# Optimization experiments

Hardware: AMD Instinct MI355X
Metric: run time of the kernel (lower is better)

The kernel has to match this reference:

```python
import jax, jax.numpy as jnp
import numpy as np

K_REP = 4          # repulsion neighbors
REP_THRESH = 0.02  # repulsion distance threshold
K_NORM = 16        # PCA-normal neighborhood size (includes self)
CD_W, REP_W, NORM_W = 1.0, 0.1, 0.01


def _pdist2(x, y):
    # squared pairwise distances: [B,N,M]
    xx = (x * x).sum(-1)
    yy = (y * y).sum(-1)
    return xx[..., :, None] + yy[..., None, :] - 2.0 * jnp.einsum('bnd,bmd->bnm', x, y)


def _gather_points(pts, idx):
    # pts: [B,N,3], idx: [B,N,k] -> [B,N,k,3]
    return jax.vmap(lambda p, i: p[i])(pts, idx)


def _pca_normals(pts):
    # normals via PCA over K_NORM nearest neighbors (self included)
    D = _pdist2(pts, pts)                       # [B,N,N]
    _, idx = jax.lax.top_k(-D, K_NORM)          # [B,N,K]
    nb = _gather_points(pts, idx)               # [B,N,K,3]
    c = nb - nb.mean(axis=-2, keepdims=True)
    cov = jnp.einsum('bnkd,bnke->bnde', c, c) / K_NORM  # [B,N,3,3]
    _, vecs = jnp.linalg.eigh(cov)              # ascending eigenvalues
    return vecs[..., :, 0]                      # eigenvector of smallest eigenvalue


def reference(pred, gt):
    # --- chamfer distance (squared, bidirectional mean) ---
    Dpg = _pdist2(pred, gt)                     # [B,N,M]
    cd = Dpg.min(axis=-1).mean() + Dpg.min(axis=-2).mean()

    # --- repulsion loss: k=4 NN on pred (excluding self) ---
    Dpp = _pdist2(pred, pred)                   # [B,N,N]
    neg_d2, _ = jax.lax.top_k(-Dpp, K_REP + 1)  # nearest incl. self
    d2 = -neg_d2[..., 1:]                       # drop self
    d = jnp.sqrt(jnp.maximum(d2, 1e-12))
    rep = jax.nn.relu(REP_THRESH - d).mean()

    # --- normal consistency via PCA normals (k=16) ---
    n_pred = _pca_normals(pred)
    n_gt = _pca_normals(gt)
    normc = 1.0 - (n_pred * n_gt).sum(-1).mean()

    return CD_W * cd + REP_W * rep + NORM_W * normc


def setup_inputs() -> dict:
    key = jax.random.key(0)
    k1, k2 = jax.random.split(key)
    B, N = 8, 2048
    pred = jax.random.uniform(k1, (B, N, 3), dtype=jnp.float32)
    gt = jax.random.uniform(k2, (B, N, 3), dtype=jnp.float32)
    return {"pred": pred, "gt": gt}
```

## Files before the change

kernel.cpp:

```cpp
#include <hip/hip_runtime.h>


#define NB 8
#define NP 2048
#define KW 10
#define KN 16
#define NQ (2 * NB * NP)


__device__ __forceinline__ float f_slapy2(float x, float y) {
    float xa = fabsf(x), ya = fabsf(y);
    float w = fmaxf(xa, ya), zm = fminf(xa, ya);
    if (zm == 0.f) return w;
    float q = zm / w;
    return w * sqrtf(1.f + q * q);
}

__device__ __forceinline__ void f_slartg(float f, float g, float* cs, float* sn, float* r) {
    if (g == 0.f) { *cs = 1.f; *sn = 0.f; *r = f; }
    else if (f == 0.f) { *cs = 0.f; *sn = copysignf(1.f, g); *r = fabsf(g); }
    else {
        float d = sqrtf(__fadd_rn(__fmul_rn(f, f), __fmul_rn(g, g)));
        *cs = fabsf(f) / d;
        *r  = copysignf(d, f);
        *sn = g / *r;
    }
}

__device__ void f_slaev2(float a, float b, float c,
                         float* rt1, float* rt2, float* cs1, float* sn1) {
    float sm = a + c;
    float df = a - c;
    float adf = fabsf(df);
    float tb = b + b;
    float ab = fabsf(tb);
    float acmx, acmn;
    if (fabsf(a) > fabsf(c)) { acmx = a; acmn = c; } else { acmx = c; acmn = a; }
    float rt;
    if (adf > ab)      { float q = ab / adf; rt = adf * sqrtf(1.f + q * q); }
    else if (adf < ab) { float q = adf / ab; rt = ab * sqrtf(1.f + q * q); }
    else               rt = ab * sqrtf(2.f);
    int sgn1;
    if (sm < 0.f) {
        *rt1 = 0.5f * (sm - rt); sgn1 = -1;
        *rt2 = (acmx / *rt1) * acmn - (b / *rt1) * b;
    } else if (sm > 0.f) {
        *rt1 = 0.5f * (sm + rt); sgn1 = 1;
        *rt2 = (acmx / *rt1) * acmn - (b / *rt1) * b;
    } else {
        *rt1 = 0.5f * rt; *rt2 = -0.5f * rt; sgn1 = 1;
    }
    float cs; int sgn2;
    if (df >= 0.f) { cs = df + rt; sgn2 = 1; }
    else           { cs = df - rt; sgn2 = -1; }
    float acs = fabsf(cs);
    if (acs > ab) {
        float ct = -tb / cs;
        *sn1 = 1.f / sqrtf(1.f + ct * ct);
        *cs1 = ct * *sn1;
    } else {
        if (ab == 0.f) { *cs1 = 1.f; *sn1 = 0.f; }
        else {
            float tn = -cs / tb;
            *cs1 = 1.f / sqrtf(1.f + tn * tn);
            *sn1 = tn * *cs1;
        }
    }
    if (sgn1 == sgn2) { float tn = *cs1; *cs1 = -*sn1; *sn1 = tn; }
}


__device__ __forceinline__ float get3(float a, float b, float c, int i) {
    return i == 0 ? a : (i == 1 ? b : c);
}
__device__ __forceinline__ void set3(float& a, float& b, float& c, int i, float v) {
    a = (i == 0) ? v : a;
    b = (i == 1) ? v : b;
    c = (i == 2) ? v : c;
}
__device__ __forceinline__ float get2(float a, float b, int i) { return i == 0 ? a : b; }
__device__ __forceinline__ void set2(float& a, float& b, int i, float v) {
    a = (i == 0) ? v : a;
    b = (i == 1) ? v : b;
}

#define DGET(i)    get3(dd0, dd1, dd2, (i))
#define DSET(i, v) set3(dd0, dd1, dd2, (i), (v))
#define EGET(i)    get2(ee0, ee1, (i))
#define ESET(i, v) set2(ee0, ee1, (i), (v))
#define ZGET(r, c)    get3(z##r##0, z##r##1, z##r##2, (c))
#define ZSET(r, c, v) set3(z##r##0, z##r##1, z##r##2, (c), (v))
#define ZROT(r, ca, cb, cc, ss) { float zt_ = ZGET(r, (ca)); float zb_ = ZGET(r, (cb)); \
    ZSET(r, (ca), (cc) * zt_ - (ss) * zb_); ZSET(r, (cb), (ss) * zt_ + (cc) * zb_); }
#define ZROT3(ca, cb, cc, ss) { ZROT(0, (ca), (cb), (cc), (ss)) ZROT(1, (ca), (cb), (cc), (ss)) ZROT(2, (ca), (cb), (cc), (ss)) }

__device__ void ssyevd3_evec0(float a00, float a10, float a20,
                              float a11, float a21, float a22,
                              float* ox, float* oy, float* oz) {
    float dd0, dd1, dd2, ee0, ee1;
    float tau = 0.f, v2 = 0.f;
    float xnorm = fabsf(a20);
    if (xnorm == 0.f) {
        tau = 0.f;
        dd0 = a00; dd1 = a11; dd2 = a22; ee0 = a10; ee1 = a21;
    } else {
        float beta = -copysignf(f_slapy2(a10, xnorm), a10);
        tau = (beta - a10) / beta;
        float inv = 1.f / (a10 - beta);
        v2 = a20 * inv;
        float x1 = tau * (a11 + a21 * v2);
        float x2 = tau * (a21 + a22 * v2);
        float alpha = -0.5f * tau * (x1 + x2 * v2);
        float w1 = x1 + alpha;
        float w2 = x2 + alpha * v2;
        float b11 = a11 - 2.f * w1;
        float b21 = a21 - v2 * w1 - w2;
        float b22 = a22 - 2.f * (v2 * w2);
        dd0 = a00; dd1 = b11; dd2 = b22; ee0 = beta; ee1 = b21;
    }
    const float eps    = 5.9604645e-08f;
    const float eps2   = eps * eps;
    const float safmin = 1.1754944e-38f;
    const float ssfmax = sqrtf(1.f / safmin) / 3.f;
    const float ssfmin = sqrtf(safmin) / eps2;
    const int n = 3, nmaxit = 90;
    float z00 = 1.f, z01 = 0.f, z02 = 0.f;
    float z10 = 0.f, z11 = 1.f, z12 = 0.f;
    float z20 = 0.f, z21 = 0.f, z22 = 1.f;
    int jtot = 0;
    int l1 = 1;

    while (true) {
        if (l1 > n) break;
        if (l1 > 1) ESET(l1 - 2, 0.f);
        int m = n;
        {
            bool found = false;
            #pragma unroll
            for (int mi = 1; mi <= 2; ++mi) {
                if (!found && mi >= l1) {
                    float tst = fabsf(EGET(mi - 1));
                    if (tst == 0.f) { m = mi; found = true; }
                    else if (tst <= (sqrtf(fabsf(DGET(mi - 1))) * sqrtf(fabsf(DGET(mi)))) * eps) {
                        ESET(mi - 1, 0.f); m = mi; found = true;
                    }
                }
            }
        }
        int l = l1, lsv = l, lend = m, lendsv = lend;
        l1 = m + 1;
        if (lend == l) continue;

        float anorm = 0.f;
        #pragma unroll
        for (int i = 1; i <= 3; ++i)
            if (i >= l && i <= lend) anorm = fmaxf(anorm, fabsf(DGET(i - 1)));
        #pragma unroll
        for (int i = 1; i <= 2; ++i)
            if (i >= l && i <= lend - 1) anorm = fmaxf(anorm, fabsf(EGET(i - 1)));
        int iscale = 0; float sclto = 1.f;
        if (anorm == 0.f) continue;
        if (anorm > ssfmax) { iscale = 1; sclto = ssfmax; }
        else if (anorm < ssfmin) { iscale = 2; sclto = ssfmin; }
        if (iscale) {
            float mul = sclto / anorm;
            #pragma unroll
            for (int i = 1; i <= 3; ++i)
                if (i >= l && i <= lend) DSET(i - 1, DGET(i - 1) * mul);
            #pragma unroll
            for (int i = 1; i <= 2; ++i)
                if (i >= l && i <= lend - 1) ESET(i - 1, EGET(i - 1) * mul);
        }
        if (fabsf(DGET(lend - 1)) < fabsf(DGET(l - 1))) { lend = lsv; l = lendsv; }

        if (lend > l) {
            while (true) {
                int mq = lend;
                if (l != lend) {
                    bool found = false;
                    #pragma unroll
                    for (int i = 1; i <= 2; ++i) {
                        if (!found && i >= l && i <= lend - 1) {
                            float ei = EGET(i - 1);
                            float tst = ei * ei;
                            if (tst <= (eps2 * fabsf(DGET(i - 1))) * fabsf(DGET(i)) + safmin) { mq = i; found = true; }
                        }
                    }
                }
                if (mq < lend) ESET(mq - 1, 0.f);
                float p = DGET(l - 1);
                if (mq == l) { DSET(l - 1, p); l = l + 1; if (l <= lend) continue; break; }
                if (mq == l + 1) {
                    float rt1, rt2, c, s;
                    f_slaev2(DGET(l - 1), EGET(l - 1), DGET(l), &rt1, &rt2, &c, &s);
                    ZROT3(l, l - 1, c, s);
                    DSET(l - 1, rt1); DSET(l, rt2); ESET(l - 1, 0.f);
                    l += 2; if (l <= lend) continue; break;
                }
                if (jtot == nmaxit) break;
                jtot++;
                float g = (DGET(l) - p) / (2.f * EGET(l - 1));
                float r = f_slapy2(g, 1.f);
                g = DGET(mq - 1) - p + EGET(l - 1) / (g + copysignf(r, g));
                float s = 1.f, c = 1.f; p = 0.f;
                float cw0 = 0.f, cw1 = 0.f, sw0 = 0.f, sw1 = 0.f;
                #pragma unroll
                for (int i = 2; i >= 1; --i) {
                    if (i <= mq - 1 && i >= l) {
                        float f = s * EGET(i - 1);
                        float b = c * EGET(i - 1);
                        f_slartg(g, f, &c, &s, &r);
                        if (i != mq - 1) ESET(i, r);
                        g = DGET(i) - p;
                        r = (DGET(i - 1) - g) * s + 2.f * c * b;
                        p = s * r;
                        DSET(i, g + p);
                        g = c * r - b;
                        set2(cw0, cw1, i - l, c);
                        set2(sw0, sw1, i - l, -s);
                    }
                }
                #pragma unroll
                for (int j = 2; j >= 1; --j) {
                    if (j <= mq - l) {
                        float cj = get2(cw0, cw1, j - 1), sj = get2(sw0, sw1, j - 1);
                        int c0 = l - 1 + (j - 1);
                        ZROT3(c0 + 1, c0, cj, sj);
                    }
                }
                DSET(l - 1, DGET(l - 1) - p);
                ESET(l - 1, g);
            }
        } else {
            while (true) {
                int mq = lend;
                if (l != lend) {
                    bool found = false;
                    #pragma unroll
                    for (int i = 3; i >= 2; --i) {
                        if (!found && i <= l && i >= lend + 1) {
                            float ei = EGET(i - 2);
                            float tst = ei * ei;
                            if (tst <= (eps2 * fabsf(DGET(i - 1))) * fabsf(DGET(i - 2)) + safmin) { mq = i; found = true; }
                        }
                    }
                }
                if (mq > lend) ESET(mq - 2, 0.f);
                float p = DGET(l - 1);
                if (mq == l) { DSET(l - 1, p); l = l - 1; if (l >= lend) continue; break; }
                if (mq == l - 1) {
                    float rt1, rt2, c, s;
                    f_slaev2(DGET(l - 2), EGET(l - 2), DGET(l - 1), &rt1, &rt2, &c, &s);
                    ZROT3(l - 1, l - 2, c, s);
                    DSET(l - 2, rt1); DSET(l - 1, rt2); ESET(l - 2, 0.f);
                    l -= 2; if (l >= lend) continue; break;
                }
                if (jtot == nmaxit) break;
                jtot++;
                float g = (DGET(l - 2) - p) / (2.f * EGET(l - 2));
                float r = f_slapy2(g, 1.f);
                g = DGET(mq - 1) - p + EGET(l - 2) / (g + copysignf(r, g));
                float s = 1.f, c = 1.f; p = 0.f;
                float cw0 = 0.f, cw1 = 0.f, sw0 = 0.f, sw1 = 0.f;
                #pragma unroll
                for (int i = 1; i <= 2; ++i) {
                    if (i >= mq && i <= l - 1) {
                        float f = s * EGET(i - 1);
                        float b = c * EGET(i - 1);
                        f_slartg(g, f, &c, &s, &r);
                        if (i != mq) ESET(i - 2, r);
                        g = DGET(i - 1) - p;
                        r = (DGET(i) - g) * s + 2.f * c * b;
                        p = s * r;
                        DSET(i - 1, g + p);
                        g = c * r - b;
                        set2(cw0, cw1, i - mq, c);
                        set2(sw0, sw1, i - mq, s);
                    }
                }
                #pragma unroll
                for (int j = 1; j <= 2; ++j) {
                    if (j <= l - mq) {
                        float cj = get2(cw0, cw1, j - 1), sj = get2(sw0, sw1, j - 1);
                        int c0 = mq - 1 + (j - 1);
                        ZROT3(c0 + 1, c0, cj, sj);
                    }
                }
                DSET(l - 1, DGET(l - 1) - p);
                ESET(l - 2, g);
            }
        }
        if (iscale) {
            float mul = anorm / sclto;
            #pragma unroll
            for (int i = 1; i <= 3; ++i)
                if (i >= lsv && i <= lendsv) DSET(i - 1, DGET(i - 1) * mul);
            #pragma unroll
            for (int i = 1; i <= 2; ++i)
                if (i >= lsv && i <= lendsv - 1) ESET(i - 1, EGET(i - 1) * mul);
        }
        if (jtot >= nmaxit) break;
    }

    #pragma unroll
    for (int ii = 2; ii <= 3; ++ii) {
        int i = ii - 1, k = i;
        float p = DGET(i - 1);
        #pragma unroll
        for (int j = ii; j <= 3; ++j)
            if (DGET(j - 1) < p) { k = j; p = DGET(j - 1); }
        if (k != i) {
            DSET(k - 1, DGET(i - 1)); DSET(i - 1, p);
            { float t0 = ZGET(0, i - 1); ZSET(0, i - 1, ZGET(0, k - 1)); ZSET(0, k - 1, t0); }
            { float t1 = ZGET(1, i - 1); ZSET(1, i - 1, ZGET(1, k - 1)); ZSET(1, k - 1, t1); }
            { float t2 = ZGET(2, i - 1); ZSET(2, i - 1, ZGET(2, k - 1)); ZSET(2, k - 1, t2); }
        }
    }
    float r0 = z00, r1 = z10, r2 = z20;
    if (tau != 0.f) {
        float sum = r1 + v2 * r2;
        r1 -= tau * sum;
        r2 -= tau * (v2 * sum);
    }
    *ox = r0; *oy = r1; *oz = r2;
}


__device__ __forceinline__ float dot_rn(float ax, float ay, float az,
                                        float bx, float by, float bz) {
    return __fadd_rn(__fadd_rn(__fmul_rn(ax, bx), __fmul_rn(ay, by)), __fmul_rn(az, bz));
}

__device__ __forceinline__ void chain10(unsigned k[KW], unsigned x) {
    unsigned t = x;
    #pragma unroll
    for (int s = 0; s < KW; ++s) {
        unsigned lo = k[s] < t ? k[s] : t;
        unsigned hi = k[s] < t ? t : k[s];
        k[s] = lo; t = hi;
    }
}
__device__ __forceinline__ void chain16(unsigned k[KN], unsigned x) {
    unsigned t = x;
    #pragma unroll
    for (int s = 0; s < KN; ++s) {
        unsigned lo = k[s] < t ? k[s] : t;
        unsigned hi = k[s] < t ? t : k[s];
        k[s] = lo; t = hi;
    }
}

__global__ __launch_bounds__(512, 4) void scan_kernel(
    const float* __restrict__ pred, const float* __restrict__ gt,
    unsigned* __restrict__ kbuf_g, float* __restrict__ mbuf_g)
{
    __shared__ float4 sHome[NP];
    __shared__ float4 sOther[NP];

    int bi = blockIdx.x;
    bool predHome = bi < NB * 32;
    int lb = predHome ? bi : bi - NB * 32;
    int b = lb >> 5;
    int tile = lb & 31;
    int tid  = threadIdx.x;
    int wave = tid >> 6;
    int lane = tid & 63;

    const float* home  = (predHome ? pred : gt) + (size_t)b * NP * 3;
    const float* other = (predHome ? gt : pred) + (size_t)b * NP * 3;

    for (int t = tid; t < NP; t += 512) {
        float hx = home[3 * t], hy = home[3 * t + 1], hz = home[3 * t + 2];
        sHome[t] = make_float4(hx, hy, hz, dot_rn(hx, hy, hz, hx, hy, hz));
        float ox = other[3 * t], oy = other[3 * t + 1], oz = other[3 * t + 2];
        sOther[t] = make_float4(ox, oy, oz, 0.f);
    }
    __syncthreads();

    int im = tile * 64 + lane;
    float4 qv = sHome[im];
    float qx = qv.x, qy = qv.y, qz = qv.z, qq = qv.w;

    unsigned keys[KW];
    #pragma unroll
    for (int s = 0; s < KW; ++s) keys[s] = 0x7F800000u | (unsigned)s;

    float minv = 1e30f;

    for (int t = 0; t < NP / 8; ++t) {
        int jj = (t << 3) | wave;
        float4 h = sHome[jj];
        float dotj = dot_rn(qx, qy, qz, h.x, h.y, h.z);
        float d2 = __fsub_rn(__fadd_rn(qq, h.w), __fmul_rn(2.f, dotj));
        chain10(keys, (__float_as_uint(d2) & 0xFFFFF800u) | (unsigned)jj);
        float4 o = sOther[jj];
        float ex = qx - o.x, ey = qy - o.y, ez = qz - o.z;
        minv = fminf(minv, fmaf(ex, ex, fmaf(ey, ey, ez * ez)));
    }

    size_t gq = (size_t)(predHome ? 0 : NB * NP) + (size_t)b * NP + im;
    #pragma unroll
    for (int s = 0; s < KW; ++s)
        kbuf_g[(size_t)(s * 8 + wave) * NQ + gq] = keys[s];
    mbuf_g[(size_t)wave * NQ + gq] = minv;
}

__global__ __launch_bounds__(1024, 4) void tail_kernel(
    const float* __restrict__ pred, const float* __restrict__ gt,
    const unsigned* __restrict__ kbuf_g, const float* __restrict__ mbuf_g,
    float* __restrict__ normals, double* __restrict__ cdpart)
{
    __shared__ double wsum[16];
    int tid = threadIdx.x;
    int wave = tid >> 6, lane = tid & 63;
    size_t gq = (size_t)blockIdx.x * 1024 + tid;

    bool predHome = gq < (size_t)(NB * NP);
    int gi = predHome ? (int)gq : (int)(gq - NB * NP);
    int b  = gi >> 11;
    int im = gi & (NP - 1);
    const float* home = (predHome ? pred : gt) + (size_t)b * NP * 3;

    float qx = home[3 * im], qy = home[3 * im + 1], qz = home[3 * im + 2];
    float qq = dot_rn(qx, qy, qz, qx, qy, qz);

    unsigned k16[KN];
    unsigned tenth[8];
    #pragma unroll
    for (int s = 0; s < KW; ++s) k16[s] = kbuf_g[(size_t)(s * 8 + 0) * NQ + gq];
    tenth[0] = k16[KW - 1];
    #pragma unroll
    for (int s = KW; s < KN; ++s) k16[s] = 0x7F800000u | (unsigned)s;

    unsigned kc[KW], kn[KW];
    #pragma unroll
    for (int s = 0; s < KW; ++s) kc[s] = kbuf_g[(size_t)(s * 8 + 1) * NQ + gq];
    #pragma unroll
    for (int w = 1; w < 8; ++w) {
        if (w < 7) {
            #pragma unroll
            for (int s = 0; s < KW; ++s) kn[s] = kbuf_g[(size_t)(s * 8 + (w + 1)) * NQ + gq];
        }
        tenth[w] = kc[KW - 1];
        #pragma unroll
        for (int s = 0; s < KW; ++s) {
            unsigned kk = kc[s];
            if (__any(kk < k16[KN - 1])) chain16(k16, kk);
        }
        if (w < 7) {
            #pragma unroll
            for (int s = 0; s < KW; ++s) kc[s] = kn[s];
        }
    }
    float minv = fminf(fminf(fminf(mbuf_g[0 * NQ + gq], mbuf_g[1 * NQ + gq]),
                             fminf(mbuf_g[2 * NQ + gq], mbuf_g[3 * NQ + gq])),
                       fminf(fminf(mbuf_g[4 * NQ + gq], mbuf_g[5 * NQ + gq]),
                             fminf(mbuf_g[6 * NQ + gq], mbuf_g[7 * NQ + gq])));

    unsigned flags = 0;
    #pragma unroll
    for (int w = 0; w < 8; ++w)
        flags |= (tenth[w] < k16[KN - 1]) ? (1u << w) : 0u;

    if (__any(flags != 0)) {
        #pragma unroll
        for (int s = 0; s < KN; ++s)
            k16[s] = flags ? (0x7F800000u | (unsigned)s) : k16[s];
        for (int w = 0; w < 8; ++w) {
            #pragma unroll
            for (int s = 0; s < KW; ++s) {
                unsigned kk = kbuf_g[(size_t)(s * 8 + w) * NQ + gq];
                bool use = (flags != 0) && !((flags >> w) & 1);
                chain16(k16, use ? kk : 0xFFFFFFFFu);
            }
        }
        for (int w = 0; w < 8; ++w) {
            if (__any((flags >> w) & 1)) {
                bool actw = ((flags >> w) & 1) != 0;
                for (int t = 0; t < NP / 8; ++t) {
                    int jj = (t << 3) | w;
                    float hx = home[3 * jj], hy = home[3 * jj + 1], hz = home[3 * jj + 2];
                    float hw = dot_rn(hx, hy, hz, hx, hy, hz);
                    float dotj = dot_rn(qx, qy, qz, hx, hy, hz);
                    float d2 = __fsub_rn(__fadd_rn(qq, hw), __fmul_rn(2.f, dotj));
                    unsigned key = (__float_as_uint(d2) & 0xFFFFF800u) | (unsigned)jj;
                    chain16(k16, actw ? key : 0xFFFFFFFFu);
                }
            }
        }
    }

    float rep = 0.0f;
    if (predHome) {
        #pragma unroll
        for (int r = 1; r <= 4; ++r) {
            float d2 = __uint_as_float(k16[r] & 0xFFFFF800u);
            float dd = sqrtf(fmaxf(d2, 1e-12f));
            rep += fmaxf(0.02f - dd, 0.0f);
        }
    }

    float sx = 0.f, sy = 0.f, sz = 0.f;
    #pragma unroll
    for (int s = 0; s < KN; ++s) {
        const float* hp = home + 3 * (size_t)(k16[s] & 0x7FFu);
        sx += hp[0]; sy += hp[1]; sz += hp[2];
    }
    float mx = sx * (1.0f / KN), my = sy * (1.0f / KN), mz = sz * (1.0f / KN);
    float cxx = 0.f, cxy = 0.f, cxz = 0.f, cyy = 0.f, cyz = 0.f, czz = 0.f;
    #pragma unroll
    for (int s = 0; s < KN; ++s) {
        const float* hp = home + 3 * (size_t)(k16[s] & 0x7FFu);
        float ax = hp[0] - mx;
        float ay = hp[1] - my;
        float az = hp[2] - mz;
        cxx += ax * ax; cxy += ax * ay; cxz += ax * az;
        cyy += ay * ay; cyz += ay * az; czz += az * az;
    }
    cxx *= (1.f / KN); cxy *= (1.f / KN); cxz *= (1.f / KN);
    cyy *= (1.f / KN); cyz *= (1.f / KN); czz *= (1.f / KN);

    float nx, ny, nz;
    ssyevd3_evec0(cxx, cxy, cxz, cyy, cyz, czz, &nx, &ny, &nz);

    normals[gq * 3 + 0] = nx;
    normals[gq * 3 + 1] = ny;
    normals[gq * 3 + 2] = nz;

    double part = (double)minv * (1.0 / (NB * NP))
                + (double)rep  * (0.1 / (NB * NP * 4));

    #pragma unroll
    for (int off = 32; off > 0; off >>= 1) part += __shfl_down(part, off);
    if (lane == 0) wsum[wave] = part;
    __syncthreads();
    if (tid == 0) {
        double t = 0.0;
        #pragma unroll
        for (int w = 0; w < 16; ++w) t += wsum[w];
        cdpart[blockIdx.x] = t;
    }
}

__global__ __launch_bounds__(64) void dot_kernel(
    const float* __restrict__ normals, double* __restrict__ dotpart)
{
    const float* nP = normals;
    const float* nG = normals + (size_t)NB * NP * 3;
    int vt = blockIdx.x * 64 + threadIdx.x;
    float s = 0.f;
    for (int i = vt; i < NB * NP; i += 1024)
        s += nP[3 * i] * nG[3 * i] + nP[3 * i + 1] * nG[3 * i + 1] + nP[3 * i + 2] * nG[3 * i + 2];
    double part = (double)s;
    #pragma unroll
    for (int off = 32; off > 0; off >>= 1) part += __shfl_down(part, off);
    if (threadIdx.x == 0) dotpart[blockIdx.x] = part;
}

__global__ __launch_bounds__(64) void fin_kernel(
    const double* __restrict__ cdpart, const double* __restrict__ dotpart,
    float* __restrict__ out)
{
    int tid = threadIdx.x;
    double c = (tid < 32) ? cdpart[tid] : 0.0;
    double d = (tid < 16) ? dotpart[tid] : 0.0;
    #pragma unroll
    for (int off = 32; off > 0; off >>= 1) {
        c += __shfl_down(c, off);
        d += __shfl_down(d, off);
    }
    if (tid == 0)
        out[0] = (float)(c - d * (0.01 / (NB * NP)) + 0.01);
}

extern "C" void kernel_launch(void* const* d_in, const int* in_sizes, int n_in,
                              void* d_out, int out_size, void* d_ws, size_t ws_size,
                              hipStream_t stream)
{
    const float* pred = (const float*)d_in[0];
    const float* gt   = (const float*)d_in[1];

    char* base = (char*)d_ws;
    float*    normals = (float*)base;
    double*   cdpart  = (double*)(base + (size_t)NQ * 3 * 4);
    double*   dotpart = cdpart + 64;
    float*    mbuf_g  = (float*)(base + (size_t)NQ * 3 * 4 + 4096);
    unsigned* kbuf_g  = (unsigned*)(base + (size_t)NQ * 3 * 4 + 4096 + (size_t)NQ * 8 * 4);

    scan_kernel<<<dim3(NB * 32 * 2), dim3(512), 0, stream>>>(pred, gt, kbuf_g, mbuf_g);
    tail_kernel<<<dim3(32), dim3(1024), 0, stream>>>(pred, gt, kbuf_g, mbuf_g, normals, cdpart);
    dot_kernel<<<dim3(16), dim3(64), 0, stream>>>(normals, dotpart);
    fin_kernel<<<dim3(1), dim3(64), 0, stream>>>(cdpart, dotpart, (float*)d_out);
}
```

Before: 194.3 us.

## Fuse normal dot-product into tail kernel and pair pred/gt points per block

The tail kernel now uses 128-thread blocks where one wave handles pred points and the other handles the matching gt points. The gt normals are exchanged through shared memory, so the normal dot product is computed in place rather than written to global memory and read back by a separate dot_kernel. This removes one kernel launch and the normals buffer. It also spreads the tail work over 256 small blocks instead of 32 large ones, giving more parallelism across CUs. The final kernel sums 256 partials, and the launch count drops from four to three.

New measurement: 186.7 us. 1.04x faster.

```diff
diff --git a/kernel.cpp b/kernel.cpp
--- a/kernel.cpp
+++ b/kernel.cpp
@@ -405,20 +405,21 @@
     mbuf_g[(size_t)wave * NQ + gq] = minv;
 }
 
-__global__ __launch_bounds__(1024, 4) void tail_kernel(
+__global__ __launch_bounds__(128) void tail_kernel(
     const float* __restrict__ pred, const float* __restrict__ gt,
     const unsigned* __restrict__ kbuf_g, const float* __restrict__ mbuf_g,
-    float* __restrict__ normals, double* __restrict__ cdpart)
+    double* __restrict__ cdpart)
 {
-    __shared__ double wsum[16];
+    __shared__ float sNG[64 * 3];
+    __shared__ double wsum[2];
     int tid = threadIdx.x;
     int wave = tid >> 6, lane = tid & 63;
-    size_t gq = (size_t)blockIdx.x * 1024 + tid;
-
-    bool predHome = gq < (size_t)(NB * NP);
-    int gi = predHome ? (int)gq : (int)(gq - NB * NP);
-    int b  = gi >> 11;
-    int im = gi & (NP - 1);
+    int i = blockIdx.x * 64 + lane;
+    bool predHome = (wave == 0);
+    size_t gq = (size_t)(predHome ? 0 : NB * NP) + (size_t)i;
+
+    int b  = i >> 11;
+    int im = i & (NP - 1);
     const float* home = (predHome ? pred : gt) + (size_t)b * NP * 3;
 
     float qx = home[3 * im], qy = home[3 * im + 1], qz = home[3 * im + 2];
@@ -523,54 +524,42 @@
     float nx, ny, nz;
     ssyevd3_evec0(cxx, cxy, cxz, cyy, cyz, czz, &nx, &ny, &nz);
 
-    normals[gq * 3 + 0] = nx;
-    normals[gq * 3 + 1] = ny;
-    normals[gq * 3 + 2] = nz;
-
-    double part = (double)minv * (1.0 / (NB * NP))
-                + (double)rep  * (0.1 / (NB * NP * 4));
+    if (!predHome) {
+        sNG[lane * 3 + 0] = nx;
+        sNG[lane * 3 + 1] = ny;
+        sNG[lane * 3 + 2] = nz;
+    }
+    __syncthreads();
+
+    double part;
+    if (predHome) {
+        float gx = sNG[lane * 3 + 0];
+        float gy = sNG[lane * 3 + 1];
+        float gz = sNG[lane * 3 + 2];
+        float dotv = nx * gx + ny * gy + nz * gz;
+        part = (double)minv * (1.0 / (NB * NP))
+             + (double)rep  * (0.1 / (NB * NP * 4))
+             - (double)dotv * (0.01 / (NB * NP));
+    } else {
+        part = (double)minv * (1.0 / (NB * NP));
+    }
 
     #pragma unroll
     for (int off = 32; off > 0; off >>= 1) part += __shfl_down(part, off);
     if (lane == 0) wsum[wave] = part;
     __syncthreads();
-    if (tid == 0) {
-        double t = 0.0;
-        #pragma unroll
-        for (int w = 0; w < 16; ++w) t += wsum[w];
-        cdpart[blockIdx.x] = t;
-    }
-}
-
-__global__ __launch_bounds__(64) void dot_kernel(
-    const float* __restrict__ normals, double* __restrict__ dotpart)
-{
-    const float* nP = normals;
-    const float* nG = normals + (size_t)NB * NP * 3;
-    int vt = blockIdx.x * 64 + threadIdx.x;
-    float s = 0.f;
-    for (int i = vt; i < NB * NP; i += 1024)
-        s += nP[3 * i] * nG[3 * i] + nP[3 * i + 1] * nG[3 * i + 1] + nP[3 * i + 2] * nG[3 * i + 2];
-    double part = (double)s;
-    #pragma unroll
-    for (int off = 32; off > 0; off >>= 1) part += __shfl_down(part, off);
-    if (threadIdx.x == 0) dotpart[blockIdx.x] = part;
+    if (tid == 0) cdpart[blockIdx.x] = wsum[0] + wsum[1];
 }
 
 __global__ __launch_bounds__(64) void fin_kernel(
-    const double* __restrict__ cdpart, const double* __restrict__ dotpart,
-    float* __restrict__ out)
+    const double* __restrict__ cdpart, float* __restrict__ out)
 {
     int tid = threadIdx.x;
-    double c = (tid < 32) ? cdpart[tid] : 0.0;
-    double d = (tid < 16) ? dotpart[tid] : 0.0;
-    #pragma unroll
-    for (int off = 32; off > 0; off >>= 1) {
-        c += __shfl_down(c, off);
-        d += __shfl_down(d, off);
-    }
+    double c = cdpart[tid] + cdpart[tid + 64] + cdpart[tid + 128] + cdpart[tid + 192];
+    #pragma unroll
+    for (int off = 32; off > 0; off >>= 1) c += __shfl_down(c, off);
     if (tid == 0)
-        out[0] = (float)(c - d * (0.01 / (NB * NP)) + 0.01);
+        out[0] = (float)(c + 0.01);
 }
 
 extern "C" void kernel_launch(void* const* d_in, const int* in_sizes, int n_in,
@@ -581,14 +570,11 @@
     const float* gt   = (const float*)d_in[1];
 
     char* base = (char*)d_ws;
-    float*    normals = (float*)base;
-    double*   cdpart  = (double*)(base + (size_t)NQ * 3 * 4);
-    double*   dotpart = cdpart + 64;
-    float*    mbuf_g  = (float*)(base + (size_t)NQ * 3 * 4 + 4096);
-    unsigned* kbuf_g  = (unsigned*)(base + (size_t)NQ * 3 * 4 + 4096 + (size_t)NQ * 8 * 4);
+    double*   cdpart = (double*)base;
+    float*    mbuf_g = (float*)(base + 4096);
+    unsigned* kbuf_g = (unsigned*)(base + 4096 + (size_t)NQ * 8 * 4);
 
     scan_kernel<<<dim3(NB * 32 * 2), dim3(512), 0, stream>>>(pred, gt, kbuf_g, mbuf_g);
-    tail_kernel<<<dim3(32), dim3(1024), 0, stream>>>(pred, gt, kbuf_g, mbuf_g, normals, cdpart);
-    dot_kernel<<<dim3(16), dim3(64), 0, stream>>>(normals, dotpart);
-    fin_kernel<<<dim3(1), dim3(64), 0, stream>>>(cdpart, dotpart, (float*)d_out);
-}
+    tail_kernel<<<dim3(256), dim3(128), 0, stream>>>(pred, gt, kbuf_g, mbuf_g, cdpart);
+    fin_kernel<<<dim3(1), dim3(64), 0, stream>>>(cdpart, (float*)d_out);
+}
```
